# Optimization experiments

Measured on AMD Instinct MI355X. Metric: run time of the kernel, lower is better.

The kernel has to match this reference:

```python
import jax, jax.numpy as jnp
from jax import lax
import numpy as np

H = 180; W = 180            # BEV map: grid_size 1440 / out_size_factor 8
CIN = 384; C = 128; K = 10  # in_channels, hidden_channel, num_classes
P = 200; NH = 8; B = 2      # num_proposals, num_heads, batch
OUT_DIMS = (2, 1, 3, 2, 2, 10)  # center, height, dim, rot, vel, heatmap


def pos2embed(pos, nf=C):
    # faithful to MFFusionHead.pos2embed (note: temperature is unused in source)
    pos = pos * (2.0 * np.pi)
    dim_t = jnp.arange(nf, dtype=pos.dtype)
    dim_t = 2.0 * jnp.floor(dim_t / 2.0) / nf + 1.0
    px = pos[..., 0, None] / dim_t
    py = pos[..., 1, None] / dim_t
    def interleave(p):
        return jnp.stack((jnp.sin(p[..., 0::2]), jnp.cos(p[..., 1::2])), axis=-1).reshape(p.shape[:-1] + (nf,))
    return jnp.concatenate((interleave(py), interleave(px)), axis=-1)  # [..., 2*nf]


def conv2d(t, w, b):
    return lax.conv_general_dilated(t, w, (1, 1), 'SAME', dimension_numbers=('NCHW', 'OIHW', 'NCHW')) + b[None, :, None, None]


def conv1d(t, w, b):
    return lax.conv_general_dilated(t, w, (1,), 'SAME', dimension_numbers=('NCH', 'OIH', 'NCH')) + b[None, :, None]


def layernorm(t, g, b):
    m = t.mean(-1, keepdims=True)
    v = ((t - m) ** 2).mean(-1, keepdims=True)
    return g * (t - m) / jnp.sqrt(v + 1e-5) + b


def mha(q, k, v, w_in, b_in, w_o, b_o):
    Bq, Lq, Cq = q.shape
    d = Cq // NH
    qh = (q @ w_in[0] + b_in[0]).reshape(Bq, Lq, NH, d)
    kh = (k @ w_in[1] + b_in[1]).reshape(Bq, -1, NH, d)
    vh = (v @ w_in[2] + b_in[2]).reshape(Bq, -1, NH, d)
    att = jax.nn.softmax(jnp.einsum('bqhd,bkhd->bhqk', qh, kh) / float(np.sqrt(d)), axis=-1)
    o = jnp.einsum('bhqk,bkhd->bqhd', att, vh).reshape(Bq, Lq, Cq)
    return o @ w_o + b_o


def _forward(x, w_shared, b_shared, w_hm1, b_hm1, g_hm1, beta_hm1, w_hm2, b_hm2,
             w_fp1, b_fp1, g_fp1, beta_fp1, w_fp2, b_fp2,
             w_be1, b_be1, w_be2, b_be2,
             w_attn_s, b_attn_s, w_out_s, b_out_s,
             w_attn_c, b_attn_c, w_out_c, b_out_c,
             ln1_g, ln1_b, ln2_g, ln2_b, ln3_g, ln3_b,
             w_ff1, b_ff1, w_ff2, b_ff2,
             w_head1, b_head1, g_head1, beta_head1, w_head2, b_head2):
    Bx = x.shape[0]
    # shared 3x3 conv over fused BEV features
    feat = conv2d(x, w_shared, b_shared)                      # [B, C, H, W]

    def head2d(w1, b1, g, be, w2, b2):
        h = conv2d(feat, w1, b1)
        h = jax.nn.relu(g[None, :, None, None] * h + be[None, :, None, None])  # BN (eval, affine) + ReLU
        return conv2d(h, w2, b2)

    dense_hm = head2d(w_hm1, b_hm1, g_hm1, beta_hm1, w_hm2, b_hm2)  # [B, K, H, W]
    frontmap = head2d(w_fp1, b_fp1, g_fp1, beta_fp1, w_fp2, b_fp2)  # [B, 1, H, W] (aux output)
    del frontmap

    # local-max NMS on detached sigmoid heatmap
    hm = jax.nn.sigmoid(lax.stop_gradient(dense_hm))
    lm = lax.reduce_window(hm, -jnp.inf, lax.max, (1, 1, 3, 3), (1, 1, 1, 1), 'SAME')
    hm = hm * (hm == lm).astype(hm.dtype)

    # top-k proposal selection across (class, position)
    _, idx = lax.top_k(hm.reshape(Bx, -1), P)                 # [B, P]
    top_idx = idx % (H * W)

    feat_flat = feat.reshape(Bx, C, H * W)

    def gather(a, i):
        return jnp.take_along_axis(a, jnp.broadcast_to(i[:, None, :], (Bx, a.shape[1], P)), axis=2)

    query_feat = gather(feat_flat, top_idx)                   # [B, C, P]
    q_hm_score = gather(hm.reshape(Bx, K, H * W), top_idx)    # [B, K, P]

    # coords_bev grid (+0.5 centers), normalized for sinusoidal embedding
    bev = jnp.stack(jnp.meshgrid(jnp.arange(H, dtype=jnp.float32) + 0.5,
                                 jnp.arange(W, dtype=jnp.float32) + 0.5,
                                 indexing='ij'), axis=-1).reshape(-1, 2)
    bev_n = bev / jnp.asarray([H, W], jnp.float32)

    def emb(p):  # bev_embedding MLP on pos2embed
        return jax.nn.relu(pos2embed(p) @ w_be1 + b_be1) @ w_be2 + b_be2

    qpe = emb(bev_n[top_idx])                                 # [B, P, C]
    kpe = emb(bev_n)[None]                                    # [1, HW, C]

    q = query_feat.transpose(0, 2, 1)                         # [B, P, C]
    mem = feat_flat.transpose(0, 2, 1)                        # [B, HW, C]

    # decoder layer: self-attn -> cross-attn to BEV -> FFN (post-norm)
    q = layernorm(q + mha(q + qpe, q + qpe, q, w_attn_s, b_attn_s, w_out_s, b_out_s), ln1_g, ln1_b)
    q = layernorm(q + mha(q + qpe, mem + kpe, mem, w_attn_c, b_attn_c, w_out_c, b_out_c), ln2_g, ln2_b)
    q = layernorm(q + jax.nn.relu(q @ w_ff1 + b_ff1) @ w_ff2 + b_ff2, ln3_g, ln3_b)

    # SeparateHead prediction (Conv1d k=3 + BN + ReLU + Conv1d)
    qc = q.transpose(0, 2, 1)                                 # [B, C, P]
    outs = []
    for i, od in enumerate(OUT_DIMS):
        h = jax.nn.relu(g_head1[i][None, :, None] * conv1d(qc, w_head1[i], b_head1[i]) + beta_head1[i][None, :, None])
        outs.append(conv1d(h, w_head2[i, :od], b_head2[i, :od]))
    outs[5] = outs[5] + q_hm_score                            # fuse gathered heatmap score into class logits
    return jnp.concatenate(outs, axis=1)                      # [B, 20, P]


def setup_inputs() -> dict:
    key = jax.random.key(0)
    ks = iter(jax.random.split(key, 60))
    def rn(shape, s=0.02):
        return jax.random.normal(next(ks), shape, jnp.float32) * s
    return dict(
        x=jax.random.normal(next(ks), (B, CIN, H, W), jnp.float32),
        w_shared=rn((C, CIN, 3, 3)), b_shared=rn((C,)),
        w_hm1=rn((C, C, 3, 3)), b_hm1=rn((C,)), g_hm1=1.0 + rn((C,)), beta_hm1=rn((C,)),
        w_hm2=rn((K, C, 3, 3)), b_hm2=rn((K,)),
        w_fp1=rn((C, C, 3, 3)), b_fp1=rn((C,)), g_fp1=1.0 + rn((C,)), beta_fp1=rn((C,)),
        w_fp2=rn((1, C, 3, 3)), b_fp2=rn((1,)),
        w_be1=rn((2 * C, C)), b_be1=rn((C,)), w_be2=rn((C, C)), b_be2=rn((C,)),
        w_attn_s=rn((3, C, C)), b_attn_s=rn((3, C)), w_out_s=rn((C, C)), b_out_s=rn((C,)),
        w_attn_c=rn((3, C, C)), b_attn_c=rn((3, C)), w_out_c=rn((C, C)), b_out_c=rn((C,)),
        ln1_g=1.0 + rn((C,)), ln1_b=rn((C,)), ln2_g=1.0 + rn((C,)), ln2_b=rn((C,)),
        ln3_g=1.0 + rn((C,)), ln3_b=rn((C,)),
        w_ff1=rn((C, 2 * C)), b_ff1=rn((2 * C,)), w_ff2=rn((2 * C, C)), b_ff2=rn((C,)),
        w_head1=rn((6, C, C, 3)), b_head1=rn((6, C)), g_head1=1.0 + rn((6, C)), beta_head1=rn((6, C)),
        w_head2=rn((6, K, C, 3)), b_head2=rn((6, K)),
    )


def reference(x, w_shared, b_shared, w_hm1, b_hm1, g_hm1, beta_hm1, w_hm2, b_hm2,
              w_fp1, b_fp1, g_fp1, beta_fp1, w_fp2, b_fp2,
              w_be1, b_be1, w_be2, b_be2,
              w_attn_s, b_attn_s, w_out_s, b_out_s,
              w_attn_c, b_attn_c, w_out_c, b_out_c,
              ln1_g, ln1_b, ln2_g, ln2_b, ln3_g, ln3_b,
              w_ff1, b_ff1, w_ff2, b_ff2,
              w_head1, b_head1, g_head1, beta_head1, w_head2, b_head2):
    return _forward(x, w_shared, b_shared, w_hm1, b_hm1, g_hm1, beta_hm1, w_hm2, b_hm2,
                    w_fp1, b_fp1, g_fp1, beta_fp1, w_fp2, b_fp2,
                    w_be1, b_be1, w_be2, b_be2,
                    w_attn_s, b_attn_s, w_out_s, b_out_s,
                    w_attn_c, b_attn_c, w_out_c, b_out_c,
                    ln1_g, ln1_b, ln2_g, ln2_b, ln3_g, ln3_b,
                    w_ff1, b_ff1, w_ff2, b_ff2,
                    w_head1, b_head1, g_head1, beta_head1, w_head2, b_head2)
```

## Files before the change

kernel.cpp:

```cpp
#include <hip/hip_runtime.h>

#define HH 180
#define WW 180
#define HWN 32400
#define CC 128
#define CINN 384
#define KK 10
#define PP 200
#define NHH 8
#define BB 2
#define NTOT 324000
#define TKBINS (1 << 18)

typedef _Float16 half8 __attribute__((ext_vector_type(8)));
typedef float f32x16 __attribute__((ext_vector_type(16)));

static __device__ __forceinline__ f32x16 MFMA16(half8 a, half8 b, f32x16 c) {
    return __builtin_amdgcn_mfma_f32_32x32x16_f16(a, b, c, 0, 0, 0);
}

__global__ void k_wsplit(const float* __restrict__ w, _Float16* __restrict__ img, int cint) {
    const int e = blockIdx.x * 256 + threadIdx.x;
    const int total = (cint / 32) * 9 * 8192;
    if (e >= total) return;
    const int ii = e & 7, cout = (e >> 3) & 127, q = (e >> 10) & 3, t = (e >> 12) & 1;
    const int bidx = e >> 13, tap = bidx % 9, ch = bidx / 9;
    const int cin = ch * 32 + q * 8 + ii;
    const float v = w[((size_t)cout * cint + cin) * 9 + tap];
    const _Float16 h = (_Float16)v;
    img[e] = (t == 0) ? h : (_Float16)((v - (float)h) * 256.f);
}

__global__ void k_wsplit_hm(const float* __restrict__ w, _Float16* __restrict__ img) {
    const int e = blockIdx.x * 256 + threadIdx.x;
    const int total = 4 * 9 * 2048;
    if (e >= total) return;
    const int ii = e & 7, co = (e >> 3) & 31, q = (e >> 8) & 3, t = (e >> 10) & 1;
    const int bidx = e >> 11, tap = bidx % 9, ch = bidx / 9;
    const int cin = ch * 32 + q * 8 + ii;
    const float v = (co < 10) ? w[((size_t)co * 128 + cin) * 9 + tap] : 0.f;
    const _Float16 h = (_Float16)v;
    img[e] = (t == 0) ? h : (_Float16)((v - (float)h) * 256.f);
}

__global__ __launch_bounds__(256) void k_xsplit(const float* __restrict__ x,
    _Float16* __restrict__ out, int CIN, int NCH)
{
    __shared__ float tile[32][184];
    const int ch = blockIdx.x, y = blockIdx.y, b = blockIdx.z;
    const int tid = threadIdx.x;
    for (int s = tid; s < 32 * 180; s += 256) {
        const int c = s / 180, px = s % 180;
        tile[c][px] = x[(((size_t)b * CIN + ch * 32 + c) * HH + y) * WW + px];
    }
    __syncthreads();
    const size_t pbase = ((((size_t)b * 180 + y) * NCH + ch) * 2) * (180 * 32);
    for (int tt = tid; tt < 1440; tt += 256) {
        const int t = tt / 720, u = tt % 720, px = u >> 2, q = u & 3;
        half8 hv;
#pragma unroll
        for (int j = 0; j < 8; ++j) {
            const float v = tile[q * 8 + j][px];
            const _Float16 h = (_Float16)v;
            hv[j] = (t == 0) ? h : (_Float16)((v - (float)h) * 256.f);
        }
        *(half8*)(out + pbase + (size_t)t * (180 * 32) + px * 32 + q * 8) = hv;
    }
}

template<int NCH, int EPI, int WRITEF, int SPLIT>
__global__ __launch_bounds__(256, 3) void k_conv(
    const _Float16* __restrict__ xs, const _Float16* __restrict__ wimg,
    const float* __restrict__ bias, const float* __restrict__ g,
    const float* __restrict__ beta, float* __restrict__ outf,
    _Float16* __restrict__ outs)
{
    __shared__ __align__(16) char sh[36992];
    const int tid = threadIdx.x;
    const int b = blockIdx.z >> 1, ch2 = blockIdx.z & 1;
    const int oy0 = blockIdx.y * 2, ox0 = blockIdx.x * 64;
    const int wave = tid >> 6, l = tid & 63;
    const int wr = wave >> 1, nh = wave & 1;
    const int l31 = l & 31, kb = l >> 5;

    f32x16 acc1[2] = {};
    f32x16 acc2[2] = {};

    int wofs[2][2];
#pragma unroll
    for (int t = 0; t < 2; ++t)
#pragma unroll
        for (int s = 0; s < 2; ++s)
            wofs[t][s] = (((t * 4) + (s * 2 + kb)) * 128 + ch2 * 64 + nh * 32 + l31) * 16;

#pragma unroll 1
    for (int ch = 0; ch < NCH; ++ch) {
        if (ch) __syncthreads();
#pragma unroll
        for (int k = 0; k < 9; ++k) {
            const int tt = tid + k * 256;
            if (tt < 2112) {
                const int seg = tt / 264, u = tt - seg * 264;
                const int t = seg >> 2, r = seg & 3;
                const int i = u >> 2, q = u & 3;
                const int gy = oy0 - 1 + r, gx = ox0 - 1 + i;
                uint4 v = {0u, 0u, 0u, 0u};
                if ((unsigned)gy < 180u && (unsigned)gx < 180u)
                    v = *(const uint4*)((const char*)xs +
                        (((((size_t)b * 180 + gy) * NCH + ch) * 2 + t) * 180 + gx) * 64 + q * 16);
                *(uint4*)(sh + ((t * 4 + r) * 4 + q) * 1056 + i * 16) = v;
            }
        }
        __syncthreads();
        const char* wb = (const char*)wimg + (size_t)ch * 9 * 16384;
#pragma unroll
        for (int tap = 0; tap < 9; ++tap) {
            const char* wt = wb + tap * 16384;
            half8 bw[2][2];
#pragma unroll
            for (int t = 0; t < 2; ++t)
#pragma unroll
                for (int s = 0; s < 2; ++s)
                    bw[t][s] = *(const half8*)(wt + wofs[t][s]);
            const int ky = tap / 3, kx = tap % 3;
            const int rr = wr + ky;
#pragma unroll
            for (int s = 0; s < 2; ++s) {
                const int q = s * 2 + kb;
                half8 ah[2], al[2];
#pragma unroll
                for (int mf = 0; mf < 2; ++mf) {
                    const int io = (mf * 32 + l31 + kx) * 16;
                    ah[mf] = *(const half8*)(sh + ((rr) * 4 + q) * 1056 + io);
                    al[mf] = *(const half8*)(sh + ((4 + rr) * 4 + q) * 1056 + io);
                }
#pragma unroll
                for (int mf = 0; mf < 2; ++mf) {
                    acc1[mf] = MFMA16(ah[mf], bw[0][s], acc1[mf]);
                    acc2[mf] = MFMA16(ah[mf], bw[1][s], acc2[mf]);
                    acc2[mf] = MFMA16(al[mf], bw[0][s], acc2[mf]);
                }
            }
        }
    }

    float* C = (float*)sh;
    const float inv256 = 1.f / 256.f;
    __syncthreads();
#pragma unroll
    for (int mf = 0; mf < 2; ++mf)
#pragma unroll
        for (int reg = 0; reg < 16; ++reg) {
            const int px = mf * 32 + (reg & 3) + 8 * (reg >> 2) + 4 * kb;
            const int co = nh * 32 + l31;
            C[(co * 2 + wr) * 72 + px] = acc1[mf][reg] + acc2[mf][reg] * inv256;
        }
    __syncthreads();
    if (WRITEF) {
        for (int tt = tid; tt < 2048; tt += 256) {
            const int co = tt >> 5, rem = tt & 31, r = rem >> 4, qx = rem & 15;
            const int gx = ox0 + qx * 4;
            if (gx < WW) {
                float4 v = *(const float4*)&C[(co * 2 + r) * 72 + qx * 4];
                const int cout = ch2 * 64 + co;
                const float bv = bias[cout];
                v.x += bv; v.y += bv; v.z += bv; v.w += bv;
                if (EPI) {
                    const float gg = g[cout], bb = beta[cout];
                    v.x = fmaxf(gg * v.x + bb, 0.f); v.y = fmaxf(gg * v.y + bb, 0.f);
                    v.z = fmaxf(gg * v.z + bb, 0.f); v.w = fmaxf(gg * v.w + bb, 0.f);
                }
                *(float4*)(outf + (((size_t)b * 128 + cout) * HH + oy0 + r) * WW + gx) = v;
            }
        }
    }
    if (SPLIT) {
        for (int tt = tid; tt < 1024; tt += 256) {
            const int q = tt & 3, px = (tt >> 2) & 63, c2 = (tt >> 8) & 1, r = tt >> 9;
            const int gx = ox0 + px;
            if (gx < WW) {
                const int chg = ch2 * 2 + c2;
                half8 hv, lv;
#pragma unroll
                for (int j = 0; j < 8; ++j) {
                    const int col = c2 * 32 + q * 8 + j;
                    const int cout = ch2 * 64 + col;
                    float v = C[(col * 2 + r) * 72 + px] + bias[cout];
                    if (EPI) v = fmaxf(g[cout] * v + beta[cout], 0.f);
                    const _Float16 h = (_Float16)v;
                    hv[j] = h;
                    lv[j] = (_Float16)((v - (float)h) * 256.f);
                }
                char* dst = (char*)outs +
                    ((((size_t)b * 180 + (oy0 + r)) * 4 + chg) * 2) * 11520 + gx * 64 + q * 16;
                *(half8*)dst = hv;
                *(half8*)(dst + 11520) = lv;
            }
        }
    }
}

template<int NCH>
__global__ __launch_bounds__(256, 3) void k_convhm2m(
    const _Float16* __restrict__ xs, const _Float16* __restrict__ wimg,
    const float* __restrict__ bias, float* __restrict__ hm_raw)
{
    __shared__ __align__(16) char sh[36992];
    const int tid = threadIdx.x;
    const int b = blockIdx.z;
    const int oy0 = blockIdx.y * 2, ox0 = blockIdx.x * 64;
    const int wave = tid >> 6, l = tid & 63;
    const int wr = wave >> 1, dup = wave & 1;
    const int l31 = l & 31, kb = l >> 5;

    f32x16 acc1[2] = {};
    f32x16 acc2[2] = {};

    const int q = dup * 2 + kb;
    int wofs[2];
#pragma unroll
    for (int t = 0; t < 2; ++t)
        wofs[t] = ((t * 4 + q) * 32 + l31) * 16;

#pragma unroll 1
    for (int ch = 0; ch < NCH; ++ch) {
        if (ch) __syncthreads();
#pragma unroll
        for (int k = 0; k < 9; ++k) {
            const int tt = tid + k * 256;
            if (tt < 2112) {
                const int seg = tt / 264, u = tt - seg * 264;
                const int t = seg >> 2, r = seg & 3;
                const int i = u >> 2, qq = u & 3;
                const int gy = oy0 - 1 + r, gx = ox0 - 1 + i;
                uint4 v = {0u, 0u, 0u, 0u};
                if ((unsigned)gy < 180u && (unsigned)gx < 180u)
                    v = *(const uint4*)((const char*)xs +
                        (((((size_t)b * 180 + gy) * NCH + ch) * 2 + t) * 180 + gx) * 64 + qq * 16);
                *(uint4*)(sh + ((t * 4 + r) * 4 + qq) * 1056 + i * 16) = v;
            }
        }
        __syncthreads();
        const char* wb = (const char*)wimg + (size_t)ch * 9 * 4096;
#pragma unroll
        for (int tap = 0; tap < 9; ++tap) {
            const char* wt = wb + tap * 4096;
            const half8 bw0 = *(const half8*)(wt + wofs[0]);
            const half8 bw1 = *(const half8*)(wt + wofs[1]);
            const int ky = tap / 3, kx = tap % 3;
            const int rr = wr + ky;
#pragma unroll
            for (int mf = 0; mf < 2; ++mf) {
                const int io = (mf * 32 + l31 + kx) * 16;
                const half8 ah = *(const half8*)(sh + ((rr) * 4 + q) * 1056 + io);
                const half8 al = *(const half8*)(sh + ((4 + rr) * 4 + q) * 1056 + io);
                acc1[mf] = MFMA16(ah, bw0, acc1[mf]);
                acc2[mf] = MFMA16(ah, bw1, acc2[mf]);
                acc2[mf] = MFMA16(al, bw0, acc2[mf]);
            }
        }
    }

    float* C = (float*)sh;
    __syncthreads();
    if (dup == 0) {
#pragma unroll
        for (int mf = 0; mf < 2; ++mf)
#pragma unroll
            for (int reg = 0; reg < 16; ++reg) {
                const int px = mf * 32 + (reg & 3) + 8 * (reg >> 2) + 4 * kb;
                C[(wr * 32 + l31) * 65 + px] = acc1[mf][reg];
                C[4160 + (wr * 32 + l31) * 65 + px] = acc2[mf][reg];
            }
    }
    __syncthreads();
    if (dup == 1 && l31 < 10) {
        const float inv256 = 1.f / 256.f;
        const float bv = bias[l31];
#pragma unroll
        for (int mf = 0; mf < 2; ++mf)
#pragma unroll
            for (int reg = 0; reg < 16; ++reg) {
                const int px = mf * 32 + (reg & 3) + 8 * (reg >> 2) + 4 * kb;
                const int gx = ox0 + px;
                if (gx < WW) {
                    const float z = (C[(wr * 32 + l31) * 65 + px] + acc1[mf][reg])
                                  + (C[4160 + (wr * 32 + l31) * 65 + px] + acc2[mf][reg]) * inv256
                                  + bv;
                    hm_raw[(((size_t)b * 10 + l31) * HH + oy0 + wr) * WW + gx] =
                        1.f / (1.f + expf(-z));
                }
            }
    }
}

__global__ void k_nms(const float* __restrict__ hm, float* __restrict__ out,
                      unsigned* __restrict__ hist) {
    int i = blockIdx.x * 256 + threadIdx.x;
    if (i >= BB * KK * HWN) return;
    int xx = i % WW, yy = (i / WW) % HH, ck = i / HWN;
    float v = hm[i], m = v;
    for (int dy = -1; dy <= 1; ++dy) {
        int ny = yy + dy;
        if ((unsigned)ny >= (unsigned)HH) continue;
        for (int dx = -1; dx <= 1; ++dx) {
            int nx = xx + dx;
            if ((unsigned)nx >= (unsigned)WW) continue;
            m = fmaxf(m, hm[(size_t)ck * HWN + ny * WW + nx]);
        }
    }
    const float mv = (v == m) ? v : 0.f;
    out[i] = mv;
    const unsigned key = __float_as_uint(mv);
    if (key != 0u)
        atomicAdd(&hist[(size_t)(i / NTOT) * TKBINS + (key >> 14)], 1u);
}

__global__ __launch_bounds__(1024) void k_tkzero(unsigned* __restrict__ hist,
                                                 unsigned* __restrict__ ccnt) {
    const int i = blockIdx.x * 1024 + threadIdx.x;
    hist[i] = 0u;
    if (i < 2) ccnt[i] = 0u;
}

__global__ __launch_bounds__(1024) void k_tkscan(const unsigned* __restrict__ hist,
                                                 unsigned* __restrict__ pivot) {
    __shared__ unsigned ls[1024];
    __shared__ unsigned s_owner, s_carry;
    const int b = blockIdx.x, t = threadIdx.x;
    const unsigned* h = hist + (size_t)b * TKBINS;
    if (t == 0) { s_owner = 0u; s_carry = 0u; pivot[b] = 0u; }
    unsigned s = 0;
    const int base = t * 256;
    for (int i = 0; i < 256; ++i) s += h[base + i];
    ls[t] = s;
    __syncthreads();
    for (int off = 1; off < 1024; off <<= 1) {
        const unsigned add = (t + off < 1024) ? ls[t + off] : 0u;
        __syncthreads();
        ls[t] += add;
        __syncthreads();
    }
    {
        const unsigned here = ls[t];
        const unsigned above = (t + 1 < 1024) ? ls[t + 1] : 0u;
        if (here >= 200u && above < 200u) { s_owner = (unsigned)t; s_carry = above; }
    }
    __syncthreads();
    const int owner = (int)s_owner;
    const unsigned carry = s_carry;
    __syncthreads();
    ls[t] = (t < 256) ? h[owner * 256 + t] : 0u;
    __syncthreads();
    for (int off = 1; off < 1024; off <<= 1) {
        const unsigned add = (t + off < 1024) ? ls[t + off] : 0u;
        __syncthreads();
        ls[t] += add;
        __syncthreads();
    }
    if (t < 256) {
        const unsigned here = carry + ls[t];
        const unsigned above = carry + ((t + 1 < 1024) ? ls[t + 1] : 0u);
        if (here >= 200u && above < 200u)
            pivot[b] = (unsigned)(owner * 256 + t) << 14;
    }
}

__global__ __launch_bounds__(1024) void k_tkcollect(const float* __restrict__ hm_msk,
    const unsigned* __restrict__ pivot, unsigned long long* __restrict__ cand,
    unsigned* __restrict__ ccnt) {
    const int b = blockIdx.y;
    const int i = blockIdx.x * 1024 + threadIdx.x;
    if (i >= NTOT) return;
    const unsigned key = __float_as_uint(hm_msk[(size_t)b * NTOT + i]);
    if (key >= pivot[b] && key != 0u) {
        const unsigned pos = atomicAdd(&ccnt[b], 1u);
        if (pos < 4096u)
            cand[(size_t)b * 4096 + pos] = (((unsigned long long)(~key)) << 32) | (unsigned)i;
    }
}

__global__ __launch_bounds__(1024) void k_tksort(const unsigned long long* __restrict__ cand,
    const unsigned* __restrict__ ccnt, int* __restrict__ top_idx) {
    __shared__ unsigned long long sb[4096];
    const int b = blockIdx.x, t = threadIdx.x;
    const unsigned cnt = ccnt[b] < 4096u ? ccnt[b] : 4096u;
    if (cnt <= 1024u) {
        sb[t] = ((unsigned)t < cnt) ? cand[(size_t)b * 4096 + t] : 0xFFFFFFFFFFFFFFFFull;
        __syncthreads();
        for (int k = 2; k <= 1024; k <<= 1) {
            for (int j = k >> 1; j > 0; j >>= 1) {
                const int ixj = t ^ j;
                if (ixj > t) {
                    const unsigned long long a = sb[t], c = sb[ixj];
                    const bool up = ((t & k) == 0);
                    if ((a > c) == up) { sb[t] = c; sb[ixj] = a; }
                }
                __syncthreads();
            }
        }
    } else {
        for (int e = t; e < 4096; e += 1024)
            sb[e] = ((unsigned)e < cnt) ? cand[(size_t)b * 4096 + e] : 0xFFFFFFFFFFFFFFFFull;
        __syncthreads();
        for (int k = 2; k <= 4096; k <<= 1) {
            for (int j = k >> 1; j > 0; j >>= 1) {
                for (int e = t; e < 4096; e += 1024) {
                    const int ixj = e ^ j;
                    if (ixj > e) {
                        const unsigned long long a = sb[e], c = sb[ixj];
                        const bool up = ((e & k) == 0);
                        if ((a > c) == up) { sb[e] = c; sb[ixj] = a; }
                    }
                }
                __syncthreads();
            }
        }
    }
    if (t < 200) top_idx[b * 200 + t] = (int)(sb[t] & 0xFFFFFFFFull) % HWN;
}

__global__ __launch_bounds__(128) void k_kpe(const float* __restrict__ w1,
    const float* __restrict__ b1, const float* __restrict__ w2,
    const float* __restrict__ b2, float* __restrict__ kpeT)
{
    __shared__ float pe[8][258];
    __shared__ float hid[8][130];
    const int tid = threadIdx.x;
    const int pos0 = blockIdx.x * 8;
    const int half = tid >> 6, m = tid & 63;
    const float dimt = 1.f + (float)m * 0.015625f;
#pragma unroll
    for (int p = 0; p < 8; ++p) {
        const int pos = pos0 + p;
        const int i = pos / WW, j = pos % WW;
        const float coord = (half == 0) ? ((float)j + 0.5f) * (1.f / 180.f)
                                        : ((float)i + 0.5f) * (1.f / 180.f);
        const float arg = (coord * 6.2831855f) / dimt;
        pe[p][half * 128 + 2 * m]     = sinf(arg);
        pe[p][half * 128 + 2 * m + 1] = cosf(arg);
    }
    __syncthreads();
    float acc[8];
#pragma unroll
    for (int p = 0; p < 8; ++p) acc[p] = b1[tid];
    for (int k = 0; k < 256; ++k) {
        const float w = w1[k * 128 + tid];
#pragma unroll
        for (int p = 0; p < 8; ++p) acc[p] += pe[p][k] * w;
    }
#pragma unroll
    for (int p = 0; p < 8; ++p) hid[p][tid] = fmaxf(acc[p], 0.f);
    __syncthreads();
#pragma unroll
    for (int p = 0; p < 8; ++p) acc[p] = b2[tid];
    for (int k = 0; k < 128; ++k) {
        const float w = w2[k * 128 + tid];
#pragma unroll
        for (int p = 0; p < 8; ++p) acc[p] += hid[p][k] * w;
    }
#pragma unroll
    for (int p = 0; p < 8; ++p) kpeT[(size_t)tid * HWN + pos0 + p] = acc[p];
}

__global__ __launch_bounds__(128) void k_gather(const float* __restrict__ feat,
    const float* __restrict__ kpeT, const float* __restrict__ hm_msk,
    const int* __restrict__ top_idx, float* __restrict__ q0,
    float* __restrict__ qpe, float* __restrict__ qhm)
{
    const int p = blockIdx.x, b = blockIdx.y, c = threadIdx.x;
    const int idx = top_idx[b * 200 + p];
    q0[((size_t)b * 200 + p) * 128 + c]  = feat[((size_t)b * 128 + c) * HWN + idx];
    qpe[((size_t)b * 200 + p) * 128 + c] = kpeT[(size_t)c * HWN + idx];
    if (c < 10)
        qhm[((size_t)b * 10 + c) * 200 + p] = hm_msk[((size_t)b * 10 + c) * HWN + idx];
}

__global__ __launch_bounds__(128) void k_proj_self(const float* __restrict__ q0,
    const float* __restrict__ qpe, const float* __restrict__ w,
    const float* __restrict__ bias, float* __restrict__ qh,
    float* __restrict__ kh, float* __restrict__ vh)
{
    __shared__ float in0[128], in1[128];
    const int p = blockIdx.x, b = blockIdx.y, c = threadIdx.x;
    const size_t base = ((size_t)b * 200 + p) * 128;
    const float a = q0[base + c], pe = qpe[base + c];
    in0[c] = a + pe; in1[c] = a;
    __syncthreads();
    float aq = bias[c], ak = bias[128 + c], av = bias[256 + c];
    for (int k = 0; k < 128; ++k) {
        const float i0 = in0[k];
        aq += i0 * w[k * 128 + c];
        ak += i0 * w[16384 + k * 128 + c];
        av += in1[k] * w[32768 + k * 128 + c];
    }
    qh[base + c] = aq; kh[base + c] = ak; vh[base + c] = av;
}

__global__ __launch_bounds__(256) void k_attn_self(const float* __restrict__ qh,
    const float* __restrict__ kh, const float* __restrict__ vh, float* __restrict__ o)
{
    __shared__ float ks[200][16], vs[200][16];
    const int h = blockIdx.x, b = blockIdx.y, tid = threadIdx.x;
    for (int s = tid; s < 3200; s += 256) {
        const int n = s >> 4, d = s & 15;
        ks[n][d] = kh[((size_t)b * 200 + n) * 128 + h * 16 + d];
        vs[n][d] = vh[((size_t)b * 200 + n) * 128 + h * 16 + d];
    }
    __syncthreads();
    if (tid < 200) {
        float q[16];
#pragma unroll
        for (int d = 0; d < 16; ++d)
            q[d] = qh[((size_t)b * 200 + tid) * 128 + h * 16 + d] * 0.25f;
        float mmax = -1e30f, lsum = 0.f, acc[16];
#pragma unroll
        for (int d = 0; d < 16; ++d) acc[d] = 0.f;
        for (int j = 0; j < 200; ++j) {
            float s = 0.f;
#pragma unroll
            for (int d = 0; d < 16; ++d) s += q[d] * ks[j][d];
            const float mn = fmaxf(mmax, s);
            const float corr = __expf(mmax - mn);
            const float pv = __expf(s - mn);
            lsum = lsum * corr + pv;
#pragma unroll
            for (int d = 0; d < 16; ++d) acc[d] = acc[d] * corr + pv * vs[j][d];
            mmax = mn;
        }
#pragma unroll
        for (int d = 0; d < 16; ++d)
            o[((size_t)b * 200 + tid) * 128 + h * 16 + d] = acc[d] / lsum;
    }
}

__global__ __launch_bounds__(128) void k_proj_ln(const float* __restrict__ src,
    const float* __restrict__ W, const float* __restrict__ bW,
    const float* __restrict__ resid, const float* __restrict__ g,
    const float* __restrict__ lb, float* __restrict__ out)
{
    __shared__ float sIn[128];
    __shared__ float rbuf[4];
    const int p = blockIdx.x, b = blockIdx.y, c = threadIdx.x;
    const size_t base = ((size_t)b * 200 + p) * 128;
    sIn[c] = src[base + c];
    __syncthreads();
    float v = bW[c] + resid[base + c];
    for (int k = 0; k < 128; ++k) v += sIn[k] * W[k * 128 + c];
    float s = v;
#pragma unroll
    for (int off = 32; off >= 1; off >>= 1) s += __shfl_xor(s, off);
    if ((c & 63) == 0) rbuf[c >> 6] = s;
    __syncthreads();
    const float mean = (rbuf[0] + rbuf[1]) * (1.f / 128.f);
    const float dv = v - mean;
    float s2 = dv * dv;
#pragma unroll
    for (int off = 32; off >= 1; off >>= 1) s2 += __shfl_xor(s2, off);
    if ((c & 63) == 0) rbuf[2 + (c >> 6)] = s2;
    __syncthreads();
    const float var = (rbuf[2] + rbuf[3]) * (1.f / 128.f);
    out[base + c] = g[c] * dv / sqrtf(var + 1e-5f) + lb[c];
}

__global__ __launch_bounds__(128) void k_proj_q(const float* __restrict__ q1n,
    const float* __restrict__ qpe, const float* __restrict__ w,
    const float* __restrict__ bw, float* __restrict__ out)
{
    __shared__ float in0[128];
    const int p = blockIdx.x, b = blockIdx.y, c = threadIdx.x;
    const size_t base = ((size_t)b * 200 + p) * 128;
    in0[c] = q1n[base + c] + qpe[base + c];
    __syncthreads();
    float a = bw[c];
    for (int k = 0; k < 128; ++k) a += in0[k] * w[k * 128 + c];
    out[base + c] = a;
}

__global__ __launch_bounds__(256) void k_kv_cross(const float* __restrict__ feat,
    const float* __restrict__ kpeT, const float* __restrict__ w,
    const float* __restrict__ bias, float* __restrict__ kh, float* __restrict__ vh)
{
    __shared__ float as[32][68];
    __shared__ float wk[32][128], wv[32][128];
    const int tid = threadIdx.x, n0 = blockIdx.x * 64, b = blockIdx.y;
    const int cg = tid & 31, ng = tid >> 5;
    float ak[4][8], av[4][8];
#pragma unroll
    for (int i = 0; i < 4; ++i)
#pragma unroll
        for (int j = 0; j < 8; ++j) { ak[i][j] = 0.f; av[i][j] = 0.f; }
    for (int kc = 0; kc < 128; kc += 32) {
        for (int s = tid; s < 2048; s += 256) {
            const int k = s >> 6, n = s & 63;
            float fv = 0.f;
            if (n0 + n < HWN)
                fv = feat[((size_t)b * 128 + kc + k) * HWN + n0 + n]
                   + kpeT[(size_t)(kc + k) * HWN + n0 + n];
            as[k][n] = fv;
        }
        for (int s = tid; s < 4096; s += 256) {
            const int k = s >> 7, c = s & 127;
            wk[k][c] = w[(128 + kc + k) * 128 + c];
            wv[k][c] = w[(256 + kc + k) * 128 + c];
        }
        __syncthreads();
#pragma unroll
        for (int k = 0; k < 32; ++k) {
            const float4 x0 = *(const float4*)&as[k][ng * 8];
            const float4 x1 = *(const float4*)&as[k][ng * 8 + 4];
            const float4 wk4 = *(const float4*)&wk[k][cg * 4];
            const float4 wv4 = *(const float4*)&wv[k][cg * 4];
            float xv[8] = {x0.x, x0.y, x0.z, x0.w, x1.x, x1.y, x1.z, x1.w};
#pragma unroll
            for (int j = 0; j < 8; ++j) {
                ak[0][j] += wk4.x * xv[j]; ak[1][j] += wk4.y * xv[j];
                ak[2][j] += wk4.z * xv[j]; ak[3][j] += wk4.w * xv[j];
                av[0][j] += wv4.x * xv[j]; av[1][j] += wv4.y * xv[j];
                av[2][j] += wv4.z * xv[j]; av[3][j] += wv4.w * xv[j];
            }
        }
        __syncthreads();
    }
    const float bk0 = bias[128 + cg * 4], bk1 = bias[128 + cg * 4 + 1];
    const float bk2 = bias[128 + cg * 4 + 2], bk3 = bias[128 + cg * 4 + 3];
    const float bv0 = bias[256 + cg * 4], bv1 = bias[256 + cg * 4 + 1];
    const float bv2 = bias[256 + cg * 4 + 2], bv3 = bias[256 + cg * 4 + 3];
#pragma unroll
    for (int j = 0; j < 8; ++j) {
        const int n = n0 + ng * 8 + j;
        if (n < HWN) {
            float4 ko = make_float4(ak[0][j] + bk0, ak[1][j] + bk1, ak[2][j] + bk2, ak[3][j] + bk3);
            float4 vo = make_float4(av[0][j] + bv0, av[1][j] + bv1, av[2][j] + bv2, av[3][j] + bv3);
            *(float4*)(kh + ((size_t)b * HWN + n) * 128 + cg * 4) = ko;
            *(float4*)(vh + ((size_t)b * HWN + n) * 128 + cg * 4) = vo;
        }
    }
}

#define KSPLIT 16
__global__ __launch_bounds__(256) void k_flash(const float* __restrict__ qh,
    const float* __restrict__ kh, const float* __restrict__ vh,
    float* __restrict__ o_part, float* __restrict__ m_part, float* __restrict__ l_part)
{
    __shared__ float ksm[64][16];
    __shared__ float vsm[64][16];
    const int bh = blockIdx.x, rt = blockIdx.y, ksid = blockIdx.z;
    const int b = bh >> 3, h = bh & 7;
    const int tid = threadIdx.x;
    const int wave = tid >> 6, lane = tid & 63;
    const int r2 = lane >> 2, qd = lane & 3;
    const int row0 = rt * 128 + wave * 32 + r2 * 2;
    float q0r[16], q1r[16];
    {
        const bool a0 = row0 < 200, a1 = row0 + 1 < 200;
#pragma unroll
        for (int d = 0; d < 16; ++d) {
            q0r[d] = a0 ? qh[((size_t)b * 200 + row0) * 128 + h * 16 + d] * 0.25f : 0.f;
            q1r[d] = a1 ? qh[((size_t)b * 200 + row0 + 1) * 128 + h * 16 + d] * 0.25f : 0.f;
        }
    }
    const int nBase = ksid * (HWN / KSPLIT), nEnd = nBase + (HWN / KSPLIT);
    float m0 = -1e30f, m1 = -1e30f, l0 = 0.f, l1 = 0.f;
    float acc0[16], acc1[16];
#pragma unroll
    for (int d = 0; d < 16; ++d) { acc0[d] = 0.f; acc1[d] = 0.f; }
    for (int c0 = nBase; c0 < nEnd; c0 += 64) {
        const int cnt = (nEnd - c0 < 64) ? (nEnd - c0) : 64;
        __syncthreads();
        {
            const int n = tid >> 2, d0 = (tid & 3) << 2;
            float4 kv = make_float4(0, 0, 0, 0), vv = make_float4(0, 0, 0, 0);
            if (n < cnt) {
                kv = *(const float4*)(kh + ((size_t)b * HWN + c0 + n) * 128 + h * 16 + d0);
                vv = *(const float4*)(vh + ((size_t)b * HWN + c0 + n) * 128 + h * 16 + d0);
            }
            *(float4*)(&ksm[n][d0]) = kv;
            *(float4*)(&vsm[n][d0]) = vv;
        }
        __syncthreads();
        float s0[16], s1[16];
        float cm0 = -1e30f, cm1 = -1e30f;
#pragma unroll
        for (int jj = 0; jj < 16; ++jj) {
            const int j = (jj << 2) | qd;
            float t0 = 0.f, t1 = 0.f;
#pragma unroll
            for (int d = 0; d < 16; ++d) {
                const float kvv = ksm[j][d];
                t0 += q0r[d] * kvv; t1 += q1r[d] * kvv;
            }
            const bool valid = j < cnt;
            t0 = valid ? t0 : -1e30f;
            t1 = valid ? t1 : -1e30f;
            s0[jj] = t0; s1[jj] = t1;
            cm0 = fmaxf(cm0, t0); cm1 = fmaxf(cm1, t1);
        }
        cm0 = fmaxf(cm0, __shfl_xor(cm0, 1)); cm0 = fmaxf(cm0, __shfl_xor(cm0, 2));
        cm1 = fmaxf(cm1, __shfl_xor(cm1, 1)); cm1 = fmaxf(cm1, __shfl_xor(cm1, 2));
        const float mn0 = fmaxf(m0, cm0), mn1 = fmaxf(m1, cm1);
        const float cr0 = __expf(m0 - mn0), cr1 = __expf(m1 - mn1);
        l0 *= cr0; l1 *= cr1;
#pragma unroll
        for (int d = 0; d < 16; ++d) { acc0[d] *= cr0; acc1[d] *= cr1; }
#pragma unroll
        for (int jj = 0; jj < 16; ++jj) {
            const int j = (jj << 2) | qd;
            const float p0 = __expf(s0[jj] - mn0);
            const float p1 = __expf(s1[jj] - mn1);
            l0 += p0; l1 += p1;
#pragma unroll
            for (int d = 0; d < 16; ++d) {
                const float vvv = vsm[j][d];
                acc0[d] += p0 * vvv; acc1[d] += p1 * vvv;
            }
        }
        m0 = mn0; m1 = mn1;
    }
    l0 += __shfl_xor(l0, 1); l0 += __shfl_xor(l0, 2);
    l1 += __shfl_xor(l1, 1); l1 += __shfl_xor(l1, 2);
#pragma unroll
    for (int d = 0; d < 16; ++d) {
        acc0[d] += __shfl_xor(acc0[d], 1); acc0[d] += __shfl_xor(acc0[d], 2);
        acc1[d] += __shfl_xor(acc1[d], 1); acc1[d] += __shfl_xor(acc1[d], 2);
    }
    if (qd == 0) {
        const size_t pbase = ((size_t)bh * KSPLIT + ksid) * 200;
        if (row0 < 200) {
#pragma unroll
            for (int d = 0; d < 16; ++d) o_part[(pbase + row0) * 16 + d] = acc0[d];
            m_part[pbase + row0] = m0; l_part[pbase + row0] = l0;
        }
        if (row0 + 1 < 200) {
#pragma unroll
            for (int d = 0; d < 16; ++d) o_part[(pbase + row0 + 1) * 16 + d] = acc1[d];
            m_part[pbase + row0 + 1] = m1; l_part[pbase + row0 + 1] = l1;
        }
    }
}

__global__ __launch_bounds__(64) void k_merge(const float* __restrict__ o_part,
    const float* __restrict__ m_part, const float* __restrict__ l_part,
    float* __restrict__ o_c)
{
    const int row = blockIdx.x, bh = blockIdx.y;
    const int b = bh >> 3, h = bh & 7;
    const int lane = threadIdx.x;
    float M = -1e30f;
#pragma unroll
    for (int k = 0; k < KSPLIT; ++k)
        M = fmaxf(M, m_part[((size_t)bh * KSPLIT + k) * 200 + row]);
    float L = 0.f;
#pragma unroll
    for (int k = 0; k < KSPLIT; ++k)
        L += l_part[((size_t)bh * KSPLIT + k) * 200 + row]
           * __expf(m_part[((size_t)bh * KSPLIT + k) * 200 + row] - M);
    if (lane < 16) {
        float o = 0.f;
#pragma unroll
        for (int k = 0; k < KSPLIT; ++k)
            o += o_part[(((size_t)bh * KSPLIT + k) * 200 + row) * 16 + lane]
               * __expf(m_part[((size_t)bh * KSPLIT + k) * 200 + row] - M);
        o_c[((size_t)b * 200 + row) * 128 + h * 16 + lane] = o / L;
    }
}

__global__ __launch_bounds__(256) void k_ffn_ln(const float* __restrict__ x,
    const float* __restrict__ w1, const float* __restrict__ b1,
    const float* __restrict__ w2, const float* __restrict__ b2,
    const float* __restrict__ g, const float* __restrict__ lb, float* __restrict__ out)
{
    __shared__ float xr[128];
    __shared__ float hs[256];
    __shared__ float rbuf[8];
    const int p = blockIdx.x, b = blockIdx.y, t = threadIdx.x;
    const size_t base = ((size_t)b * 200 + p) * 128;
    if (t < 128) xr[t] = x[base + t];
    __syncthreads();
    float hv = b1[t];
    for (int k = 0; k < 128; ++k) hv += xr[k] * w1[k * 256 + t];
    hs[t] = fmaxf(hv, 0.f);
    __syncthreads();
    float v = 0.f;
    if (t < 128) {
        v = b2[t] + xr[t];
        for (int k = 0; k < 256; ++k) v += hs[k] * w2[k * 128 + t];
    }
    float s = (t < 128) ? v : 0.f;
#pragma unroll
    for (int off = 32; off >= 1; off >>= 1) s += __shfl_xor(s, off);
    if ((t & 63) == 0) rbuf[t >> 6] = s;
    __syncthreads();
    const float mean = (rbuf[0] + rbuf[1] + rbuf[2] + rbuf[3]) * (1.f / 128.f);
    const float dv = v - mean;
    float s2 = (t < 128) ? dv * dv : 0.f;
#pragma unroll
    for (int off = 32; off >= 1; off >>= 1) s2 += __shfl_xor(s2, off);
    if ((t & 63) == 0) rbuf[4 + (t >> 6)] = s2;
    __syncthreads();
    const float var = (rbuf[4] + rbuf[5] + rbuf[6] + rbuf[7]) * (1.f / 128.f);
    if (t < 128) out[base + t] = g[t] * dv / sqrtf(var + 1e-5f) + lb[t];
}

__global__ __launch_bounds__(256) void k_head_h(const float* __restrict__ q3,
    const float* __restrict__ w1, const float* __restrict__ b1,
    const float* __restrict__ g, const float* __restrict__ beta,
    float* __restrict__ h_all)
{
    __shared__ float qw[128][32];
    const int pt = blockIdx.x, ih = blockIdx.y, b = blockIdx.z;
    const int tid = threadIdx.x;
    for (int s = tid; s < 4096; s += 256) {
        const int c = s & 127, wg = s >> 7;
        const int pg = pt * 24 - 1 + wg;
        qw[c][wg] = ((unsigned)pg < 200u) ? q3[((size_t)b * 200 + pg) * 128 + c] : 0.f;
    }
    __syncthreads();
    const int c = tid & 127, half = tid >> 7;
    float acc[12];
#pragma unroll
    for (int pp = 0; pp < 12; ++pp) acc[pp] = 0.f;
    const float* wbase = w1 + ((size_t)ih * 128 + c) * 384;
    for (int cin = 0; cin < 128; ++cin) {
        const float4* qp = (const float4*)&qw[cin][half * 12];
        const float4 a0 = qp[0], a1 = qp[1], a2 = qp[2], a3 = qp[3];
        float xr[16] = {a0.x, a0.y, a0.z, a0.w, a1.x, a1.y, a1.z, a1.w,
                        a2.x, a2.y, a2.z, a2.w, a3.x, a3.y, a3.z, a3.w};
        const float w0 = wbase[cin * 3], w1v = wbase[cin * 3 + 1], w2v = wbase[cin * 3 + 2];
#pragma unroll
        for (int pp = 0; pp < 12; ++pp)
            acc[pp] += xr[pp] * w0 + xr[pp + 1] * w1v + xr[pp + 2] * w2v;
    }
    const float bs = b1[ih * 128 + c], gg = g[ih * 128 + c], bt = beta[ih * 128 + c];
#pragma unroll
    for (int pp = 0; pp < 12; ++pp) {
        const int p = pt * 24 + half * 12 + pp;
        if (p < 200)
            h_all[(((size_t)b * 6 + ih) * 128 + c) * 200 + p] =
                fmaxf(gg * (acc[pp] + bs) + bt, 0.f);
    }
}

__global__ void k_head_out(const float* __restrict__ h_all, const float* __restrict__ w2,
    const float* __restrict__ b2, const float* __restrict__ qhm, float* __restrict__ out)
{
    const int gid = blockIdx.x * 256 + threadIdx.x;
    if (gid >= 8000) return;
    const int p = gid % 200, rem = gid / 200, row = rem % 20, b = rem / 20;
    int i, oo;
    if (row < 2)       { i = 0; oo = row; }
    else if (row < 3)  { i = 1; oo = row - 2; }
    else if (row < 6)  { i = 2; oo = row - 3; }
    else if (row < 8)  { i = 3; oo = row - 6; }
    else if (row < 10) { i = 4; oo = row - 8; }
    else               { i = 5; oo = row - 10; }
    const float* hb = h_all + (((size_t)b * 6 + i) * 128) * 200;
    const float* wb = w2 + ((size_t)i * 10 + oo) * 384;
    float acc = b2[i * 10 + oo];
    for (int c = 0; c < 128; ++c) {
        const float* hr = hb + (size_t)c * 200 + p;
        const float x0 = (p > 0) ? hr[-1] : 0.f;
        const float x1 = hr[0];
        const float x2 = (p < 199) ? hr[1] : 0.f;
        acc += x0 * wb[c * 3] + x1 * wb[c * 3 + 1] + x2 * wb[c * 3 + 2];
    }
    if (i == 5) acc += qhm[((size_t)b * 10 + oo) * 200 + p];
    out[((size_t)b * 20 + row) * 200 + p] = acc;
}

extern "C" void kernel_launch(void* const* d_in, const int* in_sizes, int n_in,
                              void* d_out, int out_size, void* d_ws, size_t ws_size,
                              hipStream_t stream) {
    (void)in_sizes; (void)n_in; (void)out_size; (void)ws_size;
    const float* x        = (const float*)d_in[0];
    const float* w_shared = (const float*)d_in[1];
    const float* b_shared = (const float*)d_in[2];
    const float* w_hm1    = (const float*)d_in[3];
    const float* b_hm1    = (const float*)d_in[4];
    const float* g_hm1    = (const float*)d_in[5];
    const float* beta_hm1 = (const float*)d_in[6];
    const float* w_hm2    = (const float*)d_in[7];
    const float* b_hm2    = (const float*)d_in[8];
    const float* w_be1    = (const float*)d_in[15];
    const float* b_be1    = (const float*)d_in[16];
    const float* w_be2    = (const float*)d_in[17];
    const float* b_be2    = (const float*)d_in[18];
    const float* w_attn_s = (const float*)d_in[19];
    const float* b_attn_s = (const float*)d_in[20];
    const float* w_out_s  = (const float*)d_in[21];
    const float* b_out_s  = (const float*)d_in[22];
    const float* w_attn_c = (const float*)d_in[23];
    const float* b_attn_c = (const float*)d_in[24];
    const float* w_out_c  = (const float*)d_in[25];
    const float* b_out_c  = (const float*)d_in[26];
    const float* ln1_g    = (const float*)d_in[27];
    const float* ln1_b    = (const float*)d_in[28];
    const float* ln2_g    = (const float*)d_in[29];
    const float* ln2_b    = (const float*)d_in[30];
    const float* ln3_g    = (const float*)d_in[31];
    const float* ln3_b    = (const float*)d_in[32];
    const float* w_ff1    = (const float*)d_in[33];
    const float* b_ff1    = (const float*)d_in[34];
    const float* w_ff2    = (const float*)d_in[35];
    const float* b_ff2    = (const float*)d_in[36];
    const float* w_head1  = (const float*)d_in[37];
    const float* b_head1  = (const float*)d_in[38];
    const float* g_head1  = (const float*)d_in[39];
    const float* bt_head1 = (const float*)d_in[40];
    const float* w_head2  = (const float*)d_in[41];
    const float* b_head2  = (const float*)d_in[42];

    char* ws = (char*)d_ws;
    size_t off = 0;
    auto alloc = [&](size_t bytes) { size_t o = off; off += (bytes + 255) & ~(size_t)255; return o; };
    _Float16* wimg_s  = (_Float16*)(ws + alloc((size_t)12*9*16384));
    _Float16* wimg_h1 = (_Float16*)(ws + alloc((size_t)4*9*16384));
    _Float16* wimg_hm = (_Float16*)(ws + alloc((size_t)4*9*2048*2));
    char*     xs1reg  = (ws + alloc((size_t)2*180*12*2*180*32*2));
    _Float16* xs1     = (_Float16*)xs1reg;
    _Float16* xs2     = (_Float16*)(ws + alloc((size_t)2*180*4*2*180*32*2));
    float* feat   = (float*)(ws + alloc((size_t)2*128*HWN*4));
    float* bufA   = (float*)(ws + alloc((size_t)2*128*HWN*4));
    float* kpeT   = (float*)(ws + alloc((size_t)128*HWN*4));
    int*   topidx = (int*)  (ws + alloc((size_t)2*200*4));
    unsigned* hist  = (unsigned*)(ws + alloc((size_t)2*TKBINS*4));
    unsigned* pivot = (unsigned*)(ws + alloc((size_t)2*4));
    unsigned long long* cand = (unsigned long long*)(ws + alloc((size_t)2*4096*8));
    unsigned* ccnt  = (unsigned*)(ws + alloc((size_t)2*4));
    float* q0     = (float*)(ws + alloc((size_t)2*200*128*4));
    float* qpe    = (float*)(ws + alloc((size_t)2*200*128*4));
    float* q_hm   = (float*)(ws + alloc((size_t)2*10*200*4));
    float* qh_s   = (float*)(ws + alloc((size_t)2*200*128*4));
    float* kh_s   = (float*)(ws + alloc((size_t)2*200*128*4));
    float* vh_s   = (float*)(ws + alloc((size_t)2*200*128*4));
    float* o_s    = (float*)(ws + alloc((size_t)2*200*128*4));
    float* q1n    = (float*)(ws + alloc((size_t)2*200*128*4));
    float* qh_c   = (float*)(ws + alloc((size_t)2*200*128*4));
    float* o_c    = (float*)(ws + alloc((size_t)2*200*128*4));
    float* q2n    = (float*)(ws + alloc((size_t)2*200*128*4));
    float* q3     = (float*)(ws + alloc((size_t)2*200*128*4));
    float* h_all  = (float*)(ws + alloc((size_t)2*6*128*200*4));

    size_t xo = 0;
    auto xalloc = [&](size_t bytes) { size_t o = xo; xo += (bytes + 255) & ~(size_t)255; return o; };
    float* bufB   = (float*)(xs1reg + xalloc((size_t)2*128*HWN*4));
    float* hm_raw = (float*)(xs1reg + xalloc((size_t)2*10*HWN*4));
    float* hm_msk = (float*)(xs1reg + xalloc((size_t)2*10*HWN*4));
    float* o_part = (float*)(xs1reg + xalloc((size_t)16*KSPLIT*200*16*4));
    float* m_part = (float*)(xs1reg + xalloc((size_t)16*KSPLIT*200*4));
    float* l_part = (float*)(xs1reg + xalloc((size_t)16*KSPLIT*200*4));
    _Float16* h1s = (_Float16*)(xs1reg + xalloc((size_t)2*180*4*2*180*32*2));

    k_tkzero<<<(2*TKBINS)/1024, 1024, 0, stream>>>(hist, ccnt);
    k_wsplit<<<(12*9*8192 + 255)/256, 256, 0, stream>>>(w_shared, wimg_s, CINN);
    k_wsplit<<<(4*9*8192 + 255)/256, 256, 0, stream>>>(w_hm1, wimg_h1, 128);
    k_wsplit_hm<<<(4*9*2048 + 255)/256, 256, 0, stream>>>(w_hm2, wimg_hm);
    k_xsplit<<<dim3(12, 180, 2), 256, 0, stream>>>(x, xs1, CINN, 12);
    k_kpe<<<HWN/8, 128, 0, stream>>>(w_be1, b_be1, w_be2, b_be2, kpeT);
    k_conv<12, 0, 1, 1><<<dim3(3, 90, 4), 256, 0, stream>>>(xs1, wimg_s, b_shared, nullptr, nullptr, feat, xs2);
    k_conv<4, 1, 0, 1><<<dim3(3, 90, 4), 256, 0, stream>>>(xs2, wimg_h1, b_hm1, g_hm1, beta_hm1, nullptr, h1s);
    k_convhm2m<4><<<dim3(3, 90, 2), 256, 0, stream>>>(h1s, wimg_hm, b_hm2, hm_raw);
    k_nms<<<(2*10*HWN + 255)/256, 256, 0, stream>>>(hm_raw, hm_msk, hist);
    k_tkscan<<<2, 1024, 0, stream>>>(hist, pivot);
    k_tkcollect<<<dim3(317, 2), 1024, 0, stream>>>(hm_msk, pivot, cand, ccnt);
    k_tksort<<<2, 1024, 0, stream>>>(cand, ccnt, topidx);
    k_gather<<<dim3(200, 2), 128, 0, stream>>>(feat, kpeT, hm_msk, topidx, q0, qpe, q_hm);
    k_proj_self<<<dim3(200, 2), 128, 0, stream>>>(q0, qpe, w_attn_s, b_attn_s, qh_s, kh_s, vh_s);
    k_attn_self<<<dim3(8, 2), 256, 0, stream>>>(qh_s, kh_s, vh_s, o_s);
    k_proj_ln<<<dim3(200, 2), 128, 0, stream>>>(o_s, w_out_s, b_out_s, q0, ln1_g, ln1_b, q1n);
    k_proj_q<<<dim3(200, 2), 128, 0, stream>>>(q1n, qpe, w_attn_c, b_attn_c, qh_c);
    k_kv_cross<<<dim3(507, 2), 256, 0, stream>>>(feat, kpeT, w_attn_c, b_attn_c, bufA, bufB);
    k_flash<<<dim3(16, 2, KSPLIT), 256, 0, stream>>>(qh_c, bufA, bufB, o_part, m_part, l_part);
    k_merge<<<dim3(200, 16), 64, 0, stream>>>(o_part, m_part, l_part, o_c);
    k_proj_ln<<<dim3(200, 2), 128, 0, stream>>>(o_c, w_out_c, b_out_c, q1n, ln2_g, ln2_b, q2n);
    k_ffn_ln<<<dim3(200, 2), 256, 0, stream>>>(q2n, w_ff1, b_ff1, w_ff2, b_ff2, ln3_g, ln3_b, q3);
    k_head_h<<<dim3(9, 6, 2), 256, 0, stream>>>(q3, w_head1, b_head1, g_head1, bt_head1, h_all);
    k_head_out<<<32, 256, 0, stream>>>(h_all, w_head2, b_head2, q_hm, (float*)d_out);
}
```

Measured before the change: 1.019 ms.

## Prefetch conv weights, raise conv occupancy, widen kpe tiles, fuse query projection

The conv kernel now loads the next tap's weight fragments from global memory while the current tap's MFMAs run, and its launch bounds ask for 4 blocks per SM instead of 3. The positional-embedding MLP kernel handles 16 positions per block instead of 8 to reuse each weight load more. The cross-attention query projection is folded into the layernorm kernel, which drops one launch and one round trip of the intermediate through global memory. The risks are register spills in the conv from the extra prefetch registers under a tighter occupancy target, and more registers per thread in the kpe kernel.

```diff
diff --git a/kernel.cpp b/kernel.cpp
--- a/kernel.cpp
+++ b/kernel.cpp
@@ -69,7 +69,7 @@
 }
 
 template<int NCH, int EPI, int WRITEF, int SPLIT>
-__global__ __launch_bounds__(256, 3) void k_conv(
+__global__ __launch_bounds__(256, 4) void k_conv(
     const _Float16* __restrict__ xs, const _Float16* __restrict__ wimg,
     const float* __restrict__ bias, const float* __restrict__ g,
     const float* __restrict__ beta, float* __restrict__ outf,
@@ -92,6 +92,13 @@
 #pragma unroll
         for (int s = 0; s < 2; ++s)
             wofs[t][s] = (((t * 4) + (s * 2 + kb)) * 128 + ch2 * 64 + nh * 32 + l31) * 16;
+
+    half8 bwC[2][2], bwN[2][2];
+#pragma unroll
+    for (int t = 0; t < 2; ++t)
+#pragma unroll
+        for (int s = 0; s < 2; ++s)
+            bwC[t][s] = *(const half8*)((const char*)wimg + wofs[t][s]);
 
 #pragma unroll 1
     for (int ch = 0; ch < NCH; ++ch) {
@@ -112,16 +119,18 @@
             }
         }
         __syncthreads();
-        const char* wb = (const char*)wimg + (size_t)ch * 9 * 16384;
 #pragma unroll
         for (int tap = 0; tap < 9; ++tap) {
-            const char* wt = wb + tap * 16384;
-            half8 bw[2][2];
-#pragma unroll
-            for (int t = 0; t < 2; ++t)
-#pragma unroll
-                for (int s = 0; s < 2; ++s)
-                    bw[t][s] = *(const half8*)(wt + wofs[t][s]);
+            const int bidx = ch * 9 + tap;
+            const bool pf = (bidx + 1 < NCH * 9);
+            if (pf) {
+                const char* wn = (const char*)wimg + (size_t)(bidx + 1) * 16384;
+#pragma unroll
+                for (int t = 0; t < 2; ++t)
+#pragma unroll
+                    for (int s = 0; s < 2; ++s)
+                        bwN[t][s] = *(const half8*)(wn + wofs[t][s]);
+            }
             const int ky = tap / 3, kx = tap % 3;
             const int rr = wr + ky;
 #pragma unroll
@@ -136,10 +145,17 @@
                 }
 #pragma unroll
                 for (int mf = 0; mf < 2; ++mf) {
-                    acc1[mf] = MFMA16(ah[mf], bw[0][s], acc1[mf]);
-                    acc2[mf] = MFMA16(ah[mf], bw[1][s], acc2[mf]);
-                    acc2[mf] = MFMA16(al[mf], bw[0][s], acc2[mf]);
+                    acc1[mf] = MFMA16(ah[mf], bwC[0][s], acc1[mf]);
+                    acc2[mf] = MFMA16(ah[mf], bwC[1][s], acc2[mf]);
+                    acc2[mf] = MFMA16(al[mf], bwC[0][s], acc2[mf]);
                 }
+            }
+            if (pf) {
+#pragma unroll
+                for (int t = 0; t < 2; ++t)
+#pragma unroll
+                    for (int s = 0; s < 2; ++s)
+                        bwC[t][s] = bwN[t][s];
             }
         }
     }
@@ -424,14 +440,14 @@
     const float* __restrict__ b1, const float* __restrict__ w2,
     const float* __restrict__ b2, float* __restrict__ kpeT)
 {
-    __shared__ float pe[8][258];
-    __shared__ float hid[8][130];
+    __shared__ float pe[16][258];
+    __shared__ float hid[16][130];
     const int tid = threadIdx.x;
-    const int pos0 = blockIdx.x * 8;
+    const int pos0 = blockIdx.x * 16;
     const int half = tid >> 6, m = tid & 63;
     const float dimt = 1.f + (float)m * 0.015625f;
 #pragma unroll
-    for (int p = 0; p < 8; ++p) {
+    for (int p = 0; p < 16; ++p) {
         const int pos = pos0 + p;
         const int i = pos / WW, j = pos % WW;
         const float coord = (half == 0) ? ((float)j + 0.5f) * (1.f / 180.f)
@@ -441,26 +457,26 @@
         pe[p][half * 128 + 2 * m + 1] = cosf(arg);
     }
     __syncthreads();
-    float acc[8];
-#pragma unroll
-    for (int p = 0; p < 8; ++p) acc[p] = b1[tid];
+    float acc[16];
+#pragma unroll
+    for (int p = 0; p < 16; ++p) acc[p] = b1[tid];
     for (int k = 0; k < 256; ++k) {
         const float w = w1[k * 128 + tid];
 #pragma unroll
-        for (int p = 0; p < 8; ++p) acc[p] += pe[p][k] * w;
-    }
-#pragma unroll
-    for (int p = 0; p < 8; ++p) hid[p][tid] = fmaxf(acc[p], 0.f);
-    __syncthreads();
-#pragma unroll
-    for (int p = 0; p < 8; ++p) acc[p] = b2[tid];
+        for (int p = 0; p < 16; ++p) acc[p] += pe[p][k] * w;
+    }
+#pragma unroll
+    for (int p = 0; p < 16; ++p) hid[p][tid] = fmaxf(acc[p], 0.f);
+    __syncthreads();
+#pragma unroll
+    for (int p = 0; p < 16; ++p) acc[p] = b2[tid];
     for (int k = 0; k < 128; ++k) {
         const float w = w2[k * 128 + tid];
 #pragma unroll
-        for (int p = 0; p < 8; ++p) acc[p] += hid[p][k] * w;
-    }
-#pragma unroll
-    for (int p = 0; p < 8; ++p) kpeT[(size_t)tid * HWN + pos0 + p] = acc[p];
+        for (int p = 0; p < 16; ++p) acc[p] += hid[p][k] * w;
+    }
+#pragma unroll
+    for (int p = 0; p < 16; ++p) kpeT[(size_t)tid * HWN + pos0 + p] = acc[p];
 }
 
 __global__ __launch_bounds__(128) void k_gather(const float* __restrict__ feat,
@@ -534,13 +550,17 @@
     }
 }
 
+template<int FUSEQ>
 __global__ __launch_bounds__(128) void k_proj_ln(const float* __restrict__ src,
     const float* __restrict__ W, const float* __restrict__ bW,
     const float* __restrict__ resid, const float* __restrict__ g,
-    const float* __restrict__ lb, float* __restrict__ out)
+    const float* __restrict__ lb, float* __restrict__ out,
+    const float* __restrict__ qpe, const float* __restrict__ wq,
+    const float* __restrict__ bq, float* __restrict__ qout)
 {
     __shared__ float sIn[128];
     __shared__ float rbuf[4];
+    __shared__ float lnrow[128];
     const int p = blockIdx.x, b = blockIdx.y, c = threadIdx.x;
     const size_t base = ((size_t)b * 200 + p) * 128;
     sIn[c] = src[base + c];
@@ -560,21 +580,15 @@
     if ((c & 63) == 0) rbuf[2 + (c >> 6)] = s2;
     __syncthreads();
     const float var = (rbuf[2] + rbuf[3]) * (1.f / 128.f);
-    out[base + c] = g[c] * dv / sqrtf(var + 1e-5f) + lb[c];
-}
-
-__global__ __launch_bounds__(128) void k_proj_q(const float* __restrict__ q1n,
-    const float* __restrict__ qpe, const float* __restrict__ w,
-    const float* __restrict__ bw, float* __restrict__ out)
-{
-    __shared__ float in0[128];
-    const int p = blockIdx.x, b = blockIdx.y, c = threadIdx.x;
-    const size_t base = ((size_t)b * 200 + p) * 128;
-    in0[c] = q1n[base + c] + qpe[base + c];
-    __syncthreads();
-    float a = bw[c];
-    for (int k = 0; k < 128; ++k) a += in0[k] * w[k * 128 + c];
-    out[base + c] = a;
+    const float ln = g[c] * dv / sqrtf(var + 1e-5f) + lb[c];
+    out[base + c] = ln;
+    if (FUSEQ) {
+        lnrow[c] = ln + qpe[base + c];
+        __syncthreads();
+        float a = bq[c];
+        for (int k = 0; k < 128; ++k) a += lnrow[k] * wq[k * 128 + c];
+        qout[base + c] = a;
+    }
 }
 
 __global__ __launch_bounds__(256) void k_kv_cross(const float* __restrict__ feat,
@@ -956,7 +970,7 @@
     k_wsplit<<<(4*9*8192 + 255)/256, 256, 0, stream>>>(w_hm1, wimg_h1, 128);
     k_wsplit_hm<<<(4*9*2048 + 255)/256, 256, 0, stream>>>(w_hm2, wimg_hm);
     k_xsplit<<<dim3(12, 180, 2), 256, 0, stream>>>(x, xs1, CINN, 12);
-    k_kpe<<<HWN/8, 128, 0, stream>>>(w_be1, b_be1, w_be2, b_be2, kpeT);
+    k_kpe<<<HWN/16, 128, 0, stream>>>(w_be1, b_be1, w_be2, b_be2, kpeT);
     k_conv<12, 0, 1, 1><<<dim3(3, 90, 4), 256, 0, stream>>>(xs1, wimg_s, b_shared, nullptr, nullptr, feat, xs2);
     k_conv<4, 1, 0, 1><<<dim3(3, 90, 4), 256, 0, stream>>>(xs2, wimg_h1, b_hm1, g_hm1, beta_hm1, nullptr, h1s);
     k_convhm2m<4><<<dim3(3, 90, 2), 256, 0, stream>>>(h1s, wimg_hm, b_hm2, hm_raw);
@@ -967,12 +981,13 @@
     k_gather<<<dim3(200, 2), 128, 0, stream>>>(feat, kpeT, hm_msk, topidx, q0, qpe, q_hm);
     k_proj_self<<<dim3(200, 2), 128, 0, stream>>>(q0, qpe, w_attn_s, b_attn_s, qh_s, kh_s, vh_s);
     k_attn_self<<<dim3(8, 2), 256, 0, stream>>>(qh_s, kh_s, vh_s, o_s);
-    k_proj_ln<<<dim3(200, 2), 128, 0, stream>>>(o_s, w_out_s, b_out_s, q0, ln1_g, ln1_b, q1n);
-    k_proj_q<<<dim3(200, 2), 128, 0, stream>>>(q1n, qpe, w_attn_c, b_attn_c, qh_c);
+    k_proj_ln<1><<<dim3(200, 2), 128, 0, stream>>>(o_s, w_out_s, b_out_s, q0, ln1_g, ln1_b, q1n,
+                                                   qpe, w_attn_c, b_attn_c, qh_c);
     k_kv_cross<<<dim3(507, 2), 256, 0, stream>>>(feat, kpeT, w_attn_c, b_attn_c, bufA, bufB);
     k_flash<<<dim3(16, 2, KSPLIT), 256, 0, stream>>>(qh_c, bufA, bufB, o_part, m_part, l_part);
     k_merge<<<dim3(200, 16), 64, 0, stream>>>(o_part, m_part, l_part, o_c);
-    k_proj_ln<<<dim3(200, 2), 128, 0, stream>>>(o_c, w_out_c, b_out_c, q1n, ln2_g, ln2_b, q2n);
+    k_proj_ln<0><<<dim3(200, 2), 128, 0, stream>>>(o_c, w_out_c, b_out_c, q1n, ln2_g, ln2_b, q2n,
+                                                   nullptr, nullptr, nullptr, nullptr);
     k_ffn_ln<<<dim3(200, 2), 256, 0, stream>>>(q2n, w_ff1, b_ff1, w_ff2, b_ff2, ln3_g, ln3_b, q3);
     k_head_h<<<dim3(9, 6, 2), 256, 0, stream>>>(q3, w_head1, b_head1, g_head1, bt_head1, h_all);
     k_head_out<<<32, 256, 0, stream>>>(h_all, w_head2, b_head2, q_hm, (float*)d_out);
```

Result: slower. 1.101 ms (+8.0%).
